# Optimization experiments

Measured on AMD Instinct MI355X. Metric: run time of the kernel, lower is better.

Reference implementation:

```python
import jax, jax.numpy as jnp
import numpy as np

NUM_HEADS = 6
KERNEL = 5
EPS = 1e-6


def _neighbor_idx(L, k):
    # NATTEN neighborhood: window start clamped so every query has exactly k neighbors
    starts = jnp.clip(jnp.arange(L) - k // 2, 0, L - k)
    return starts[:, None] + jnp.arange(k)  # [L, k]


def ada_rmsnorm(x, scale, w1, b1, w2, b2):
    # x: [B,C,D,H,W]; RMS over spatial dims, gamma from channel means via small MLP
    rms = jnp.sqrt(jnp.mean(x * x, axis=(2, 3, 4), keepdims=True) + EPS)
    xn = x / rms
    stats = jnp.mean(x, axis=(2, 3, 4))                 # [B,C]
    h = jax.nn.relu(stats @ w1.T + b1)                  # [B,2C]
    gamma = jax.nn.sigmoid(h @ w2.T + b2)               # [B,C]
    return xn * (scale * gamma[:, :, None, None, None])


def reference(x, scale1, n1_w1, n1_b1, n1_w2, n1_b2,
              qkv_w, qkv_b, proj_w, proj_b,
              scale2, n2_w1, n2_b1, n2_w2, n2_b2,
              mlp_w1, mlp_b1, mlp_w2, mlp_b2):
    B, C, D, H, W = x.shape
    nh_, k_ = NUM_HEADS, KERNEL
    hd = C // nh_
    K3 = k_ ** 3

    # --- norm1 + neighborhood attention ---
    h = ada_rmsnorm(x, scale1, n1_w1, n1_b1, n1_w2, n1_b2)
    t = jnp.transpose(h, (0, 2, 3, 4, 1))               # [B,D,H,W,C]
    qkv = t @ qkv_w.T + qkv_b                           # [B,D,H,W,3C]
    q, k, v = jnp.split(qkv, 3, axis=-1)
    q = q.reshape(B, D, H, W, nh_, hd)
    k = k.reshape(B, D, H, W, nh_, hd)
    v = v.reshape(B, D, H, W, nh_, hd)

    iD = _neighbor_idx(D, k_)
    iH = _neighbor_idx(H, k_)
    iW = _neighbor_idx(W, k_)
    nd = iD[:, None, None, :, None, None]               # [D,1,1,k,1,1]
    nhh = iH[None, :, None, None, :, None]              # [1,H,1,1,k,1]
    nw = iW[None, None, :, None, None, :]               # [1,1,W,1,1,k]

    k_nb = k[:, nd, nhh, nw].reshape(B, D, H, W, K3, nh_, hd)
    v_nb = v[:, nd, nhh, nw].reshape(B, D, H, W, K3, nh_, hd)

    scale_qk = hd ** -0.5
    scores = jnp.einsum('bdhwnc,bdhwknc->bdhwnk', q, k_nb) * scale_qk  # [B,D,H,W,heads,K3]
    p = jax.nn.softmax(scores, axis=-1)
    o = jnp.einsum('bdhwnk,bdhwknc->bdhwnc', p, v_nb).reshape(B, D, H, W, C)
    o = o @ proj_w.T + proj_b                            # output projection
    x = x + jnp.transpose(o, (0, 4, 1, 2, 3))

    # --- norm2 + 1x1-conv MLP (GELU exact) ---
    h2 = ada_rmsnorm(x, scale2, n2_w1, n2_b1, n2_w2, n2_b2)
    m = jnp.einsum('oc,bcdhw->bodhw', mlp_w1, h2) + mlp_b1[None, :, None, None, None]
    m = jax.nn.gelu(m, approximate=False)
    m = jnp.einsum('oc,bcdhw->bodhw', mlp_w2, m) + mlp_b2[None, :, None, None, None]
    return x + m


def setup_inputs() -> dict:
    key = jax.random.key(0)
    ks = jax.random.split(key, 16)
    B, C, D, H, W = 1, 192, 16, 16, 16
    hid = 2 * C
    mlp_h = int(4.0 * C)
    s = 0.02
    inp = {
        'x': jax.random.normal(ks[0], (B, C, D, H, W), jnp.float32),
        'scale1': jnp.ones((1, C, 1, 1, 1), jnp.float32),
        'n1_w1': jax.random.normal(ks[1], (hid, C), jnp.float32) * s,
        'n1_b1': jnp.zeros((hid,), jnp.float32),
        'n1_w2': jax.random.normal(ks[2], (C, hid), jnp.float32) * s,
        'n1_b2': jnp.zeros((C,), jnp.float32),
        'qkv_w': jax.random.normal(ks[3], (3 * C, C), jnp.float32) * s,
        'qkv_b': jnp.zeros((3 * C,), jnp.float32),
        'proj_w': jax.random.normal(ks[4], (C, C), jnp.float32) * s,
        'proj_b': jnp.zeros((C,), jnp.float32),
        'scale2': jnp.ones((1, C, 1, 1, 1), jnp.float32),
        'n2_w1': jax.random.normal(ks[5], (hid, C), jnp.float32) * s,
        'n2_b1': jnp.zeros((hid,), jnp.float32),
        'n2_w2': jax.random.normal(ks[6], (C, hid), jnp.float32) * s,
        'n2_b2': jnp.zeros((C,), jnp.float32),
        'mlp_w1': jax.random.normal(ks[7], (mlp_h, C), jnp.float32) * s,
        'mlp_b1': jnp.zeros((mlp_h,), jnp.float32),
        'mlp_w2': jax.random.normal(ks[8], (C, mlp_h), jnp.float32) * s,
        'mlp_b2': jnp.zeros((C,), jnp.float32),
    }
    return inp
```

## Files before the change

### kernel.cpp

```cpp
#include <hip/hip_runtime.h>
#include <hip/hip_bf16.h>
#include <cmath>


#define NPOS 4096
#define C_CH 192
#define NB   512

typedef __bf16 bf16x8 __attribute__((ext_vector_type(8)));
typedef __bf16 bf16x4 __attribute__((ext_vector_type(4)));
typedef float  f32x4  __attribute__((ext_vector_type(4)));

__device__ __forceinline__ float bflo(unsigned int u) {
    union { unsigned int i; float f; } c; c.i = u << 16; return c.f;
}
__device__ __forceinline__ float bfhi(unsigned int u) {
    union { unsigned int i; float f; } c; c.i = u & 0xffff0000u; return c.f;
}


__device__ __forceinline__ void pre_sync(unsigned* bar, int grp) {
    __syncthreads();
    if (threadIdx.x == 0) {
        unsigned* arr    = bar + 128 + grp * 16;
        unsigned* master = bar + 256;
        unsigned* go     = bar + 272 + grp * 16;
        unsigned prev = __hip_atomic_fetch_add(arr, 1u, __ATOMIC_RELAXED,
                                               __HIP_MEMORY_SCOPE_AGENT);
        if (prev == 63u) {
            __hip_atomic_fetch_add(master, 1u, __ATOMIC_RELAXED,
                                   __HIP_MEMORY_SCOPE_AGENT);
            while (__hip_atomic_load(master, __ATOMIC_RELAXED,
                                     __HIP_MEMORY_SCOPE_AGENT) < 8u)
                __builtin_amdgcn_s_sleep(2);
            __hip_atomic_store(go, 1u, __ATOMIC_RELAXED, __HIP_MEMORY_SCOPE_AGENT);
        }
        while (__hip_atomic_load(go, __ATOMIC_RELAXED,
                                 __HIP_MEMORY_SCOPE_AGENT) == 0u)
            __builtin_amdgcn_s_sleep(2);
    }
    __syncthreads();
}

__device__ __forceinline__ void grid_sync(unsigned* bar, int idx, int xcc,
                                          unsigned myPop, unsigned nx) {
    __syncthreads();
    if (threadIdx.x == 0) {
        unsigned* base   = bar + 512 + idx * 512;
        unsigned* arr    = base + xcc * 16;
        unsigned* master = base + 128;
        unsigned* go     = base + 144 + xcc * 16;
        unsigned prev = __hip_atomic_fetch_add(arr, 1u, __ATOMIC_RELAXED,
                                               __HIP_MEMORY_SCOPE_AGENT);
        if (prev == myPop - 1u) {
            __hip_atomic_fetch_add(master, 1u, __ATOMIC_RELEASE,
                                   __HIP_MEMORY_SCOPE_AGENT);
            while (__hip_atomic_load(master, __ATOMIC_RELAXED,
                                     __HIP_MEMORY_SCOPE_AGENT) < nx)
                __builtin_amdgcn_s_sleep(2);
            __hip_atomic_store(go, 1u, __ATOMIC_RELAXED, __HIP_MEMORY_SCOPE_AGENT);
        }
        while (__hip_atomic_load(go, __ATOMIC_RELAXED,
                                 __HIP_MEMORY_SCOPE_AGENT) == 0u)
            __builtin_amdgcn_s_sleep(2);
    }
    __syncthreads();
}

__device__ __forceinline__ void conv_unit(const float* __restrict__ src,
                                          __bf16* __restrict__ dst, int base)
{
    int i = (base * 256 + (int)threadIdx.x) * 4;
    float4 v = *(const float4*)(src + i);
    bf16x4 o = { (__bf16)v.x, (__bf16)v.y, (__bf16)v.z, (__bf16)v.w };
    *(bf16x4*)(dst + i) = o;
}

__device__ void stats_unit(float* sm, const float* __restrict__ x,
                           float* __restrict__ sums, float* __restrict__ sumsq, int c)
{
    const float4* xc = (const float4*)(x + (size_t)c * NPOS);
    float a = 0.f, a2 = 0.f;
    for (int i = threadIdx.x; i < NPOS / 4; i += 256) {
        float4 v = xc[i];
        a  += v.x + v.y + v.z + v.w;
        a2 += v.x * v.x + v.y * v.y + v.z * v.z + v.w * v.w;
    }
    #pragma unroll
    for (int off = 32; off > 0; off >>= 1) {
        a  += __shfl_down(a, off);
        a2 += __shfl_down(a2, off);
    }
    float* ls = sm; float* ls2 = sm + 4;
    int wid = threadIdx.x >> 6;
    if ((threadIdx.x & 63) == 0) { ls[wid] = a; ls2[wid] = a2; }
    __syncthreads();
    if (threadIdx.x == 0) {
        float t = 0.f, t2 = 0.f;
        #pragma unroll
        for (int w = 0; w < 4; w++) { t += ls[w]; t2 += ls2[w]; }
        sums[c] = t; sumsq[c] = t2;
    }
    __syncthreads();
}

__device__ void transpose_unit(float* sm, const float* __restrict__ x,
                               __bf16* __restrict__ xb, int p0)
{
    float* lds = sm;
    int t = threadIdx.x;
    for (int idx = t; idx < 192 * 4; idx += 256) {
        int row = idx >> 2, p4 = idx & 3;
        float4 v = *(const float4*)(x + (size_t)row * NPOS + p0 + p4 * 4);
        lds[row * 17 + p4 * 4 + 0] = v.x;
        lds[row * 17 + p4 * 4 + 1] = v.y;
        lds[row * 17 + p4 * 4 + 2] = v.z;
        lds[row * 17 + p4 * 4 + 3] = v.w;
    }
    __syncthreads();
    for (int idx = t; idx < 48 * 16; idx += 256) {
        int c4 = idx >> 4, p = idx & 15;
        bf16x4 o;
        #pragma unroll
        for (int j = 0; j < 4; j++) o[j] = (__bf16)lds[(c4 * 4 + j) * 17 + p];
        *(bf16x4*)(xb + (size_t)(p0 + p) * 192 + c4 * 4) = o;
    }
    __syncthreads();
}

__device__ void compute_gsl(float* scratch, float* gslOut,
    const float* __restrict__ sums, const float* __restrict__ sumsq,
    const float* __restrict__ scale,
    const __bf16* __restrict__ w1b, const float* __restrict__ b1,
    const __bf16* __restrict__ w2b, const float* __restrict__ b2)
{
    float* stats = scratch;
    float* h     = scratch + 192;
    int t = threadIdx.x;
    if (t < C_CH)
        stats[t] = __hip_atomic_load((const float*)&sums[t], __ATOMIC_RELAXED,
                                     __HIP_MEMORY_SCOPE_AGENT) * (1.0f / (float)NPOS);
    __syncthreads();
    for (int j = t; j < 384; j += 256) {
        float acc = b1[j];
        const __bf16* wr = w1b + (size_t)j * C_CH;
        #pragma unroll 4
        for (int c = 0; c < C_CH; c += 8) {
            bf16x8 w8 = *(const bf16x8*)(wr + c);
            acc += (float)w8[0] * stats[c]     + (float)w8[1] * stats[c + 1]
                 + (float)w8[2] * stats[c + 2] + (float)w8[3] * stats[c + 3]
                 + (float)w8[4] * stats[c + 4] + (float)w8[5] * stats[c + 5]
                 + (float)w8[6] * stats[c + 6] + (float)w8[7] * stats[c + 7];
        }
        h[j] = fmaxf(acc, 0.0f);
    }
    __syncthreads();
    if (t < C_CH) {
        float acc = b2[t];
        const __bf16* wr = w2b + (size_t)t * 384;
        #pragma unroll 4
        for (int j = 0; j < 384; j += 8) {
            bf16x8 w8 = *(const bf16x8*)(wr + j);
            acc += (float)w8[0] * h[j]     + (float)w8[1] * h[j + 1]
                 + (float)w8[2] * h[j + 2] + (float)w8[3] * h[j + 3]
                 + (float)w8[4] * h[j + 4] + (float)w8[5] * h[j + 5]
                 + (float)w8[6] * h[j + 6] + (float)w8[7] * h[j + 7];
        }
        float g = 1.0f / (1.0f + __expf(-acc));
        float sq = __hip_atomic_load((const float*)&sumsq[t], __ATOMIC_RELAXED,
                                     __HIP_MEMORY_SCOPE_AGENT);
        float rms = sqrtf(sq * (1.0f / (float)NPOS) + 1e-6f);
        gslOut[t] = scale[t] * g / rms;
    }
    __syncthreads();
}

template <int K, int EPI, bool SCALEA>
__device__ void gemm_tile(__bf16* al, __bf16* bl, const float* gslLds,
    int bx, int by,
    const __bf16* __restrict__ W, const float* __restrict__ bias,
    const __bf16* __restrict__ X, void* __restrict__ out,
    const float* __restrict__ resid, int M, __bf16* __restrict__ out_kv,
    float* __restrict__ s2sum, float* __restrict__ s2sq,
    __bf16* __restrict__ xb2o)
{
    constexpr int KC  = 192;
    constexpr int LDA = 200;
    int t    = threadIdx.x;
    int lane = t & 63;
    int wv   = t >> 6;
    int r16  = lane & 15;
    int quad = lane >> 4;
    int wvm  = wv >> 1;
    int wvn  = wv & 1;
    int mBase = by * 64;
    int nBase = bx * 64;

    f32x4 acc[2][2];
    #pragma unroll
    for (int i = 0; i < 2; i++)
        #pragma unroll
        for (int j = 0; j < 2; j++)
            acc[i][j] = (f32x4){0.f, 0.f, 0.f, 0.f};

    for (int k0 = 0; k0 < K; k0 += KC) {
        #pragma unroll
        for (int it = 0; it < 6; it++) {
            int c = it * 256 + t;
            int row = c / 24, off = c - row * 24;
            bf16x8 va = *(const bf16x8*)(W + (size_t)(mBase + row) * K + k0 + off * 8);
            if (SCALEA) {
                #pragma unroll
                for (int j = 0; j < 8; j++)
                    va[j] = (__bf16)((float)va[j] * gslLds[off * 8 + j]);
            }
            *(bf16x8*)(al + row * LDA + off * 8) = va;
            bf16x8 vb = *(const bf16x8*)(X + (size_t)(nBase + row) * K + k0 + off * 8);
            *(bf16x8*)(bl + row * LDA + off * 8) = vb;
        }
        __syncthreads();
        #pragma unroll
        for (int ks = 0; ks < KC / 32; ks++) {
            bf16x8 a0 = *(const bf16x8*)(al + (wvm * 32 + r16) * LDA + ks * 32 + quad * 8);
            bf16x8 a1 = *(const bf16x8*)(al + (wvm * 32 + 16 + r16) * LDA + ks * 32 + quad * 8);
            bf16x8 b0 = *(const bf16x8*)(bl + (wvn * 32 + r16) * LDA + ks * 32 + quad * 8);
            bf16x8 b1 = *(const bf16x8*)(bl + (wvn * 32 + 16 + r16) * LDA + ks * 32 + quad * 8);
            acc[0][0] = __builtin_amdgcn_mfma_f32_16x16x32_bf16(a0, b0, acc[0][0], 0, 0, 0);
            acc[0][1] = __builtin_amdgcn_mfma_f32_16x16x32_bf16(a0, b1, acc[0][1], 0, 0, 0);
            acc[1][0] = __builtin_amdgcn_mfma_f32_16x16x32_bf16(a1, b0, acc[1][0], 0, 0, 0);
            acc[1][1] = __builtin_amdgcn_mfma_f32_16x16x32_bf16(a1, b1, acc[1][1], 0, 0, 0);
        }
        __syncthreads();
    }

    #pragma unroll
    for (int rt = 0; rt < 2; rt++) {
        int m0 = mBase + wvm * 32 + rt * 16 + quad * 4;
        float b0 = bias[m0], b1v = bias[m0 + 1], b2v = bias[m0 + 2], b3v = bias[m0 + 3];
        float ss[4] = {0.f, 0.f, 0.f, 0.f}, sq[4] = {0.f, 0.f, 0.f, 0.f};
        #pragma unroll
        for (int ct = 0; ct < 2; ct++) {
            int n = nBase + wvn * 32 + ct * 16 + r16;
            f32x4 a4 = acc[rt][ct];
            float g0 = a4[0] + b0, g1 = a4[1] + b1v, g2 = a4[2] + b2v, g3 = a4[3] + b3v;
            if (EPI == 0) {
                int sect = m0 / 192;
                int o0 = m0 - sect * 192;
                if (sect == 0) {
                    const float qs = 0.17677669529663687f;
                    *(float4*)((float*)out + (size_t)n * 192 + o0) =
                        make_float4(g0 * qs, g1 * qs, g2 * qs, g3 * qs);
                } else {
                    bf16x4 kvv = { (__bf16)g0, (__bf16)g1, (__bf16)g2, (__bf16)g3 };
                    *(bf16x4*)(out_kv + (size_t)n * 384 + (o0 >> 2) * 8 + (sect - 1) * 4) = kvv;
                }
            } else if (EPI == 2 || EPI == 4) {
                float* o = (float*)out;
                size_t i0 = (size_t)m0 * NPOS + n;
                float v0 = g0 + resid[i0];
                float v1 = g1 + resid[i0 + NPOS];
                float v2 = g2 + resid[i0 + 2 * NPOS];
                float v3 = g3 + resid[i0 + 3 * NPOS];
                o[i0] = v0; o[i0 + NPOS] = v1; o[i0 + 2 * NPOS] = v2; o[i0 + 3 * NPOS] = v3;
                if (EPI == 4) {
                    bf16x4 xv = { (__bf16)v0, (__bf16)v1, (__bf16)v2, (__bf16)v3 };
                    *(bf16x4*)(xb2o + (size_t)n * 192 + m0) = xv;
                    ss[0] += v0; sq[0] += v0 * v0;
                    ss[1] += v1; sq[1] += v1 * v1;
                    ss[2] += v2; sq[2] += v2 * v2;
                    ss[3] += v3; sq[3] += v3 * v3;
                }
            } else {
                bf16x4 v;
                v[0] = (__bf16)(0.5f * g0 * (1.0f + erff(g0 * 0.7071067811865475f)));
                v[1] = (__bf16)(0.5f * g1 * (1.0f + erff(g1 * 0.7071067811865475f)));
                v[2] = (__bf16)(0.5f * g2 * (1.0f + erff(g2 * 0.7071067811865475f)));
                v[3] = (__bf16)(0.5f * g3 * (1.0f + erff(g3 * 0.7071067811865475f)));
                *(bf16x4*)((__bf16*)out + (size_t)n * M + m0) = v;
            }
        }
        if (EPI == 4) {
            #pragma unroll
            for (int j = 0; j < 4; j++) {
                float s = ss[j], s2v = sq[j];
                #pragma unroll
                for (int off = 8; off >= 1; off >>= 1) {
                    s   += __shfl_down(s, off);
                    s2v += __shfl_down(s2v, off);
                }
                if (r16 == 0) {
                    atomicAdd(&s2sum[m0 + j], s);
                    atomicAdd(&s2sq[m0 + j], s2v);
                }
            }
        }
    }
}

__device__ __forceinline__ void attn_unit(const float* __restrict__ q,
    const __bf16* __restrict__ kv, __bf16* __restrict__ o, int unit)
{
    int t = threadIdx.x;
    int pairIdx = unit * 8 + (t >> 5);
    int sg   = (t >> 3) & 3;
    int lane = t & 7;
    int pos = pairIdx / 6;
    int head = pairIdx - pos * 6;
    int wq = pos & 15;
    int hq = (pos >> 4) & 15;
    int dq = pos >> 8;
    int d0 = min(max(dq - 2, 0), 11);
    int h0 = min(max(hq - 2, 0), 11);
    int w0 = min(max(wq - 2, 0), 11);

    const __bf16* kvb = kv + head * 64 + lane * 8;
    float4 q4 = *(const float4*)(q + (size_t)pos * 192 + head * 32 + lane * 4);

    float l = 0.0f;
    float4 acc = make_float4(0.f, 0.f, 0.f, 0.f);

    for (int dh = sg; dh < 25; dh += 4) {
        int di = dh / 5;
        int hi = dh - di * 5;
        int np0 = (d0 + di) * 256 + (h0 + hi) * 16 + w0;
        const __bf16* p = kvb + (size_t)np0 * 384;
        #pragma unroll
        for (int wi = 0; wi < 5; wi++) {
            uint4 u = *(const uint4*)p;
            float s = q4.x * bflo(u.x) + q4.y * bfhi(u.x)
                    + q4.z * bflo(u.y) + q4.w * bfhi(u.y);
            s += __shfl_xor(s, 1);
            s += __shfl_xor(s, 2);
            s += __shfl_xor(s, 4);
            float pr = __expf(s);
            l += pr;
            acc.x += pr * bflo(u.z);
            acc.y += pr * bfhi(u.z);
            acc.z += pr * bflo(u.w);
            acc.w += pr * bfhi(u.w);
            p += 384;
        }
    }

    #pragma unroll
    for (int off = 8; off <= 16; off <<= 1) {
        l     += __shfl_xor(l, off);
        acc.x += __shfl_xor(acc.x, off);
        acc.y += __shfl_xor(acc.y, off);
        acc.z += __shfl_xor(acc.z, off);
        acc.w += __shfl_xor(acc.w, off);
    }

    if (sg == 0) {
        float rl = 1.0f / l;
        bf16x4 ov = { (__bf16)(acc.x * rl), (__bf16)(acc.y * rl),
                      (__bf16)(acc.z * rl), (__bf16)(acc.w * rl) };
        *(bf16x4*)(o + (size_t)pos * 192 + head * 32 + lane * 4) = ov;
    }
}

__global__ __launch_bounds__(256) void fused(
    const float* __restrict__ x, const float* __restrict__ scale1,
    const float* __restrict__ n1_w1, const float* __restrict__ n1_b1,
    const float* __restrict__ n1_w2, const float* __restrict__ n1_b2,
    const float* __restrict__ qkv_w, const float* __restrict__ qkv_b,
    const float* __restrict__ proj_w, const float* __restrict__ proj_b,
    const float* __restrict__ scale2,
    const float* __restrict__ n2_w1, const float* __restrict__ n2_b1,
    const float* __restrict__ n2_w2, const float* __restrict__ n2_b2,
    const float* __restrict__ mlp_w1, const float* __restrict__ mlp_b1,
    const float* __restrict__ mlp_w2, const float* __restrict__ mlp_b2,
    float* __restrict__ ws, float* __restrict__ x2)
{
    __shared__ __align__(16) char smraw[52224];
    __bf16* al     = (__bf16*)smraw;
    __bf16* bl     = al + 64 * 200;
    float*  smf    = (float*)smraw;
    float*  gslLds = (float*)(smraw + 51200);

    float*  q_buf   = ws;
    __bf16* kv_buf  = (__bf16*)(ws + 786432);
    __bf16* xb      = (__bf16*)(ws + 2359296);
    __bf16* o_attn  = (__bf16*)(ws + 2752512);
    __bf16* qkv_wb  = (__bf16*)(ws + 3145728);
    __bf16* proj_wb = qkv_wb + 110592;
    __bf16* m1_wb   = proj_wb + 36864;
    __bf16* m2_wb   = m1_wb + 147456;
    float*  sums1   = ws + 3366912;
    float*  sumsq1  = ws + 3367104;
    float*  sums2   = ws + 3367296;
    float*  sumsq2  = ws + 3367488;
    __bf16* n1w1b   = (__bf16*)(ws + 3367680);
    __bf16* n1w2b   = n1w1b + 73728;
    __bf16* n2w1b   = n1w2b + 73728;
    __bf16* n2w2b   = n2w1b + 73728;
    unsigned* bar   = (unsigned*)(ws + 3515136);
    __bf16* m_buf   = (__bf16*)(ws + 3520512);
    __bf16* xb2     = (__bf16*)(ws + 5093376);

    int bid = blockIdx.x;
    int t   = threadIdx.x;

    int xcc = __builtin_amdgcn_s_getreg(63508) & 7;

    if (t == 0)
        __hip_atomic_fetch_add(bar + xcc * 16, 1u, __ATOMIC_RELAXED,
                               __HIP_MEMORY_SCOPE_AGENT);
    pre_sync(bar, bid & 7);
    unsigned myPop = 0, nx = 0;
    if (t == 0) {
        myPop = __hip_atomic_load(bar + xcc * 16, __ATOMIC_RELAXED,
                                  __HIP_MEMORY_SCOPE_AGENT);
        #pragma unroll
        for (int xi = 0; xi < 8; xi++)
            nx += (__hip_atomic_load(bar + xi * 16, __ATOMIC_RELAXED,
                                     __HIP_MEMORY_SCOPE_AGENT) > 0u) ? 1u : 0u;
    }

    for (int u = bid; u < 1169; u += NB) {
        if      (u < 108)  conv_unit(qkv_w,  qkv_wb, u);
        else if (u < 144)  conv_unit(proj_w, proj_wb, u - 108);
        else if (u < 288)  conv_unit(mlp_w1, m1_wb, u - 144);
        else if (u < 432)  conv_unit(mlp_w2, m2_wb, u - 288);
        else if (u < 504)  conv_unit(n1_w1,  n1w1b, u - 432);
        else if (u < 576)  conv_unit(n1_w2,  n1w2b, u - 504);
        else if (u < 648)  conv_unit(n2_w1,  n2w1b, u - 576);
        else if (u < 720)  conv_unit(n2_w2,  n2w2b, u - 648);
        else if (u < 912)  stats_unit(smf, x, sums1, sumsq1, u - 720);
        else if (u == 912) {
            if (t < 192) {
                __hip_atomic_store(&sums2[t], 0.f, __ATOMIC_RELAXED,
                                   __HIP_MEMORY_SCOPE_AGENT);
                __hip_atomic_store(&sumsq2[t], 0.f, __ATOMIC_RELAXED,
                                   __HIP_MEMORY_SCOPE_AGENT);
            }
        }
        else               transpose_unit(smf, x, xb, (u - 913) * 16);
    }
    grid_sync(bar, 0, xcc, myPop, nx);

    compute_gsl(smf, gslLds, sums1, sumsq1, scale1, n1w1b, n1_b1, n1w2b, n1_b2);
    for (int tile = bid; tile < 576; tile += NB)
        gemm_tile<192, 0, true>(al, bl, gslLds, tile & 63, tile >> 6,
                                qkv_wb, qkv_b, xb, (void*)q_buf,
                                nullptr, 576, kv_buf, nullptr, nullptr, nullptr);
    grid_sync(bar, 1, xcc, myPop, nx);

    {
        int base = (bid & 7) * 384 + (bid >> 3) * 6;
        for (int i = 0; i < 6; i++)
            attn_unit(q_buf, kv_buf, o_attn, base + i);
    }
    grid_sync(bar, 2, xcc, myPop, nx);

    if (bid < 192)
        gemm_tile<192, 4, false>(al, bl, nullptr, bid & 63, bid >> 6,
                                 proj_wb, proj_b, o_attn, (void*)x2,
                                 x, 192, nullptr, sums2, sumsq2, xb2);
    grid_sync(bar, 3, xcc, myPop, nx);

    compute_gsl(smf, gslLds, sums2, sumsq2, scale2, n2w1b, n2_b1, n2w2b, n2_b2);
    for (int tile = bid; tile < 768; tile += NB)
        gemm_tile<192, 3, true>(al, bl, gslLds, tile & 63, tile >> 6,
                                m1_wb, mlp_b1, xb2, (void*)m_buf,
                                nullptr, 768, nullptr, nullptr, nullptr, nullptr);
    grid_sync(bar, 4, xcc, myPop, nx);

    if (bid < 192)
        gemm_tile<768, 2, false>(al, bl, nullptr, bid & 63, bid >> 6,
                                 m2_wb, mlp_b2, m_buf, (void*)x2,
                                 x2, 192, nullptr, nullptr, nullptr, nullptr);
}

extern "C" void kernel_launch(void* const* d_in, const int* in_sizes, int n_in,
                              void* d_out, int out_size, void* d_ws, size_t ws_size,
                              hipStream_t stream)
{
    const float* x      = (const float*)d_in[0];
    const float* scale1 = (const float*)d_in[1];
    const float* n1_w1  = (const float*)d_in[2];
    const float* n1_b1  = (const float*)d_in[3];
    const float* n1_w2  = (const float*)d_in[4];
    const float* n1_b2  = (const float*)d_in[5];
    const float* qkv_w  = (const float*)d_in[6];
    const float* qkv_b  = (const float*)d_in[7];
    const float* proj_w = (const float*)d_in[8];
    const float* proj_b = (const float*)d_in[9];
    const float* scale2 = (const float*)d_in[10];
    const float* n2_w1  = (const float*)d_in[11];
    const float* n2_b1  = (const float*)d_in[12];
    const float* n2_w2  = (const float*)d_in[13];
    const float* n2_b2  = (const float*)d_in[14];
    const float* mlp_w1 = (const float*)d_in[15];
    const float* mlp_b1 = (const float*)d_in[16];
    const float* mlp_w2 = (const float*)d_in[17];
    const float* mlp_b2 = (const float*)d_in[18];

    float* ws = (float*)d_ws;
    float* x2 = (float*)d_out;

    hipMemsetAsync(ws + 3515136, 0, 3072 * sizeof(unsigned), stream);

    fused<<<NB, 256, 0, stream>>>(x, scale1, n1_w1, n1_b1, n1_w2, n1_b2,
                                  qkv_w, qkv_b, proj_w, proj_b,
                                  scale2, n2_w1, n2_b1, n2_w2, n2_b2,
                                  mlp_w1, mlp_b1, mlp_w2, mlp_b2,
                                  ws, x2);
}
```

Measured before the change: 205.7 us.

## Compute neighborhood attention with MFMA over shared 4x4x4 query-block K/V tiles

```diff
diff --git a/kernel.cpp b/kernel.cpp
--- a/kernel.cpp
+++ b/kernel.cpp
@@ -10,14 +10,6 @@
 typedef __bf16 bf16x8 __attribute__((ext_vector_type(8)));
 typedef __bf16 bf16x4 __attribute__((ext_vector_type(4)));
 typedef float  f32x4  __attribute__((ext_vector_type(4)));
-
-__device__ __forceinline__ float bflo(unsigned int u) {
-    union { unsigned int i; float f; } c; c.i = u << 16; return c.f;
-}
-__device__ __forceinline__ float bfhi(unsigned int u) {
-    union { unsigned int i; float f; } c; c.i = u & 0xffff0000u; return c.f;
-}
-
 
 __device__ __forceinline__ void pre_sync(unsigned* bar, int grp) {
     __syncthreads();
@@ -297,65 +289,113 @@
     }
 }
 
-__device__ __forceinline__ void attn_unit(const float* __restrict__ q,
-    const __bf16* __restrict__ kv, __bf16* __restrict__ o, int unit)
-{
+__device__ void attn_mfma(char* smbase, const float* __restrict__ q,
+                          const __bf16* __restrict__ kv, __bf16* __restrict__ o,
+                          int pb, int head)
+{
+    __bf16* Qs = (__bf16*)smbase;
+    __bf16* Ks = Qs + 64 * 40;
+    __bf16* Vt = Ks + 128 * 40;
+    __bf16* Ps = Vt + 32 * 136;
+
     int t = threadIdx.x;
-    int pairIdx = unit * 8 + (t >> 5);
-    int sg   = (t >> 3) & 3;
-    int lane = t & 7;
-    int pos = pairIdx / 6;
-    int head = pairIdx - pos * 6;
-    int wq = pos & 15;
-    int hq = (pos >> 4) & 15;
-    int dq = pos >> 8;
-    int d0 = min(max(dq - 2, 0), 11);
-    int h0 = min(max(hq - 2, 0), 11);
-    int w0 = min(max(wq - 2, 0), 11);
-
-    const __bf16* kvb = kv + head * 64 + lane * 8;
-    float4 q4 = *(const float4*)(q + (size_t)pos * 192 + head * 32 + lane * 4);
-
-    float l = 0.0f;
-    float4 acc = make_float4(0.f, 0.f, 0.f, 0.f);
-
-    for (int dh = sg; dh < 25; dh += 4) {
-        int di = dh / 5;
-        int hi = dh - di * 5;
-        int np0 = (d0 + di) * 256 + (h0 + hi) * 16 + w0;
-        const __bf16* p = kvb + (size_t)np0 * 384;
-        #pragma unroll
-        for (int wi = 0; wi < 5; wi++) {
-            uint4 u = *(const uint4*)p;
-            float s = q4.x * bflo(u.x) + q4.y * bfhi(u.x)
-                    + q4.z * bflo(u.y) + q4.w * bfhi(u.y);
-            s += __shfl_xor(s, 1);
-            s += __shfl_xor(s, 2);
-            s += __shfl_xor(s, 4);
-            float pr = __expf(s);
-            l += pr;
-            acc.x += pr * bflo(u.z);
-            acc.y += pr * bfhi(u.z);
-            acc.z += pr * bflo(u.w);
-            acc.w += pr * bfhi(u.w);
-            p += 384;
-        }
-    }
-
+    int wave = t >> 6, lane = t & 63, r16 = lane & 15, quad = lane >> 4;
+
+    int Db = (pb >> 4) * 4, Hb = ((pb >> 2) & 3) * 4, Wb = (pb & 3) * 4;
+    int r0d = min(max(Db - 2, 0), 8);
+    int r0h = min(max(Hb - 2, 0), 8);
+    int r0w = min(max(Wb - 2, 0), 8);
+
+    for (int idx = t; idx < 512; idx += 256) {
+        int qr = idx >> 3, c4 = (idx & 7) * 4;
+        int pos = (Db + (qr >> 4)) * 256 + (Hb + ((qr >> 2) & 3)) * 16 + (Wb + (qr & 3));
+        float4 v = *(const float4*)(q + (size_t)pos * 192 + head * 32 + c4);
+        bf16x4 b = { (__bf16)v.x, (__bf16)v.y, (__bf16)v.z, (__bf16)v.w };
+        *(bf16x4*)(Qs + qr * 40 + c4) = b;
+    }
+
+    int d0q = min(max(Db + wave - 2, 0), 11);
+    int h0q = min(max(Hb + quad - 2, 0), 11);
+    unsigned wm[4];
     #pragma unroll
-    for (int off = 8; off <= 16; off <<= 1) {
-        l     += __shfl_xor(l, off);
-        acc.x += __shfl_xor(acc.x, off);
-        acc.y += __shfl_xor(acc.y, off);
-        acc.z += __shfl_xor(acc.z, off);
-        acc.w += __shfl_xor(acc.w, off);
-    }
-
-    if (sg == 0) {
-        float rl = 1.0f / l;
-        bf16x4 ov = { (__bf16)(acc.x * rl), (__bf16)(acc.y * rl),
-                      (__bf16)(acc.z * rl), (__bf16)(acc.w * rl) };
-        *(bf16x4*)(o + (size_t)pos * 192 + head * 32 + lane * 4) = ov;
+    for (int reg = 0; reg < 4; reg++) {
+        int w0q = min(max(Wb + reg - 2, 0), 11);
+        unsigned m = 0;
+        #pragma unroll
+        for (int wk = 0; wk < 8; wk++) {
+            int wa = r0w + wk;
+            if (wa >= w0q && wa < w0q + 5) m |= (1u << wk);
+        }
+        wm[reg] = m;
+    }
+
+    float lpart[4] = {0.f, 0.f, 0.f, 0.f};
+    f32x4 accO[2] = { (f32x4){0.f,0.f,0.f,0.f}, (f32x4){0.f,0.f,0.f,0.f} };
+    int rowbase = wave * 16;
+
+    for (int c = 0; c < 4; c++) {
+        __syncthreads();
+        for (int idx = t; idx < 1024; idx += 256) {
+            int l128 = idx >> 3, cp = idx & 7;
+            int pos = (r0d + c * 2 + (l128 >> 6)) * 256
+                    + (r0h + ((l128 >> 3) & 7)) * 16 + (r0w + (l128 & 7));
+            uint4 u = *(const uint4*)(kv + (size_t)pos * 384 + head * 64 + cp * 8);
+            uint2 kk; kk.x = u.x; kk.y = u.y;
+            *(uint2*)(Ks + l128 * 40 + cp * 4) = kk;
+            unsigned short* vt0 = (unsigned short*)(Vt + (cp * 4) * 136 + l128);
+            vt0[0]         = (unsigned short)(u.z & 0xffff);
+            vt0[136]       = (unsigned short)(u.z >> 16);
+            vt0[272]       = (unsigned short)(u.w & 0xffff);
+            vt0[408]       = (unsigned short)(u.w >> 16);
+        }
+        __syncthreads();
+        bf16x8 aq = *(const bf16x8*)(Qs + (rowbase + r16) * 40 + quad * 8);
+        #pragma unroll
+        for (int tn = 0; tn < 8; tn++) {
+            bf16x8 bk = *(const bf16x8*)(Ks + (tn * 16 + r16) * 40 + quad * 8);
+            f32x4 sc = __builtin_amdgcn_mfma_f32_16x16x32_bf16(
+                           aq, bk, (f32x4){0.f,0.f,0.f,0.f}, 0, 0, 0);
+            int local = tn * 16 + r16;
+            int dka = r0d + c * 2 + (local >> 6);
+            int hka = r0h + ((local >> 3) & 7);
+            int wk  = local & 7;
+            bool vdh = (dka >= d0q) && (dka < d0q + 5) &&
+                       (hka >= h0q) && (hka < h0q + 5);
+            #pragma unroll
+            for (int reg = 0; reg < 4; reg++) {
+                bool v = vdh && ((wm[reg] >> wk) & 1u);
+                float p = v ? __expf(sc[reg]) : 0.f;
+                lpart[reg] += p;
+                Ps[(rowbase + quad * 4 + reg) * 136 + local] = (__bf16)p;
+            }
+        }
+        __syncthreads();
+        #pragma unroll
+        for (int tn = 0; tn < 2; tn++) {
+            #pragma unroll
+            for (int ks = 0; ks < 4; ks++) {
+                bf16x8 pa = *(const bf16x8*)(Ps + (rowbase + r16) * 136 + ks * 32 + quad * 8);
+                bf16x8 bv = *(const bf16x8*)(Vt + (tn * 16 + r16) * 136 + ks * 32 + quad * 8);
+                accO[tn] = __builtin_amdgcn_mfma_f32_16x16x32_bf16(pa, bv, accO[tn], 0, 0, 0);
+            }
+        }
+    }
+
+    #pragma unroll
+    for (int reg = 0; reg < 4; reg++) {
+        #pragma unroll
+        for (int off = 1; off < 16; off <<= 1)
+            lpart[reg] += __shfl_xor(lpart[reg], off);
+    }
+    #pragma unroll
+    for (int tn = 0; tn < 2; tn++) {
+        #pragma unroll
+        for (int reg = 0; reg < 4; reg++) {
+            int qr = rowbase + quad * 4 + reg;
+            int pos = (Db + (qr >> 4)) * 256 + (Hb + ((qr >> 2) & 3)) * 16 + (Wb + (qr & 3));
+            o[(size_t)pos * 192 + head * 32 + tn * 16 + r16] =
+                (__bf16)(accO[tn][reg] / lpart[reg]);
+        }
     }
 }
 
@@ -446,11 +486,8 @@
                                 nullptr, 576, kv_buf, nullptr, nullptr, nullptr);
     grid_sync(bar, 1, xcc, myPop, nx);
 
-    {
-        int base = (bid & 7) * 384 + (bid >> 3) * 6;
-        for (int i = 0; i < 6; i++)
-            attn_unit(q_buf, kv_buf, o_attn, base + i);
-    }
+    if (bid < 384)
+        attn_mfma(smraw, q_buf, kv_buf, o_attn, bid / 6, bid % 6);
     grid_sync(bar, 2, xcc, myPop, nx);
 
     if (bid < 192)
```

New measurement: 192.8 us. -6.2%, faster.
